# Optimization experiments

Measured on AMD Instinct MI355X. Metric: run time of the kernel, lower is better.

The kernel has to match this reference:

```python
import jax, jax.numpy as jnp
import numpy as np
from jax import lax

# Hyperparameters mirroring init_kwargs
W_DATA = 0.75
W_SMOOTH = 0.25
W_KNN = 0.5
W_BQ = 0.5
K_KNN = 32
K_BQ = 64
RADIUS = 0.75
P_NORM = 1  # loss_norm


def _sqdist(pc):
    # pc: [B,N,3] -> [B,N,N] squared pairwise distances
    x2 = jnp.sum(pc * pc, axis=-1)
    d = x2[:, :, None] + x2[:, None, :] - 2.0 * jnp.einsum('bnc,bmc->bnm', pc, pc)
    return jnp.maximum(d, 0.0)


def _group(flow, idx):
    # flow: [B,3,N], idx: [B,N,K] -> [B,3,N,K]
    return jax.vmap(lambda f, i: f[:, i])(flow, idx)


def _neighbor_loss(flow, idx):
    # flow: [B,3,N]; (flow_i - flow_j).norm(p, dim=channel).mean(K).mean()
    nn_flow = _group(flow, idx)                    # [B,3,N,K]
    diff = flow[:, :, :, None] - nn_flow           # [B,3,N,K]
    if P_NORM == 1:
        n = jnp.sum(jnp.abs(diff), axis=1)         # [B,N,K]
    else:
        n = jnp.sum(jnp.abs(diff) ** P_NORM, axis=1) ** (1.0 / P_NORM)
    return jnp.mean(jnp.mean(n, axis=-1))


def _knn_idx(sqd):
    # k nearest (self included); if dist > radius, replace with nearest index
    neg_vals, idx = lax.top_k(-sqd, K_KNN)         # [B,N,K]
    dist = jnp.sqrt(jnp.maximum(-neg_vals, 0.0))
    tmp = idx[:, :, 0:1]
    return jnp.where(dist > RADIUS, tmp, idx)


def _ballq_idx(sqd):
    # first K_BQ indices (in index order) with sqdist < radius^2, padded by first hit
    N = sqd.shape[-1]
    ar = jnp.arange(N, dtype=jnp.int32)
    keys = jnp.where(sqd < RADIUS * RADIUS, ar[None, None, :], N)  # [B,N,N]
    vals = -lax.top_k(-keys, K_BQ)[0]              # K smallest keys -> [B,N,K]
    first = vals[:, :, 0:1]
    return jnp.where(vals == N, first, vals)


def setup_inputs() -> dict:
    key = jax.random.key(0)
    k1, k2, k3, k4 = jax.random.split(key, 4)
    B, N = 4, 8192
    return {
        'pc_source': jax.random.normal(k1, (B, N, 3), dtype=jnp.float32),
        'pc_target': jax.random.normal(k2, (B, N, 3), dtype=jnp.float32),
        'pred_flow': jax.random.normal(k3, (B, N, 3), dtype=jnp.float32),
        'gt_flow': jax.random.normal(k4, (B, N, 3), dtype=jnp.float32),
        'i': 0,
    }


def reference(pc_source, pc_target, pred_flow, gt_flow, i):
    # data term: L1
    data_loss = jnp.mean(jnp.abs(pred_flow - gt_flow))
    # smoothness term
    flow = jnp.transpose(pred_flow, (0, 2, 1))     # [B,3,N]
    sqd = _sqdist(pc_source)                       # [B,N,N]
    knn_loss = _neighbor_loss(flow, _knn_idx(sqd))
    bq_loss = _neighbor_loss(flow, _ballq_idx(sqd))
    smooth = W_KNN * knn_loss + W_BQ * bq_loss
    return W_DATA * data_loss + W_SMOOTH * smooth
```

## Files before the change

### kernel.cpp

```cpp
#include <hip/hip_runtime.h>
#include <hip/hip_bf16.h>
#include <hip/hip_fp16.h>

#define NPTS 8192
#define NB 4
#define R2C 0.5625f
#define BSC (64.0f/0.5625f)
#define RPW 2
#define WPB 4
#define NGRP 256
#define NUNITS (NB*NPTS/RPW)
#define GPB (NPTS/RPW)
#define NBLK 2048
#define NCTR 64
#define UPC (NUNITS/NCTR)
#define CSTRIDE 32

typedef unsigned char u8;
typedef unsigned u32;
typedef unsigned long long u64;

__device__ __forceinline__ float wsum(float v){
#pragma unroll
  for (int o=32;o>0;o>>=1) v += __shfl_xor(v,o,64);
  return v;
}
__device__ __forceinline__ float rfl(float v){
  return __int_as_float(__builtin_amdgcn_readfirstlane(__float_as_int(v)));
}
__device__ __forceinline__ int cellof(float x,float y,float z){
  int ix=min(15,max(0,(int)((x+5.f)*1.6f)));
  int iy=min(15,max(0,(int)((y+5.f)*1.6f)));
  int iz=min(15,max(0,(int)((z+5.f)*1.6f)));
  int sx=(ix&1)|((ix&2)<<2)|((ix&4)<<4)|((ix&8)<<6);
  int sy=(iy&1)|((iy&2)<<2)|((iy&4)<<4)|((iy&8)<<6);
  int sz=(iz&1)|((iz&2)<<2)|((iz&4)<<4)|((iz&8)<<6);
  return (sx<<2)|(sy<<1)|sz;
}
__device__ __forceinline__ u32 om(float f){
  u32 u=__float_as_uint(f);
  return (u&0x80000000u)? ~u : (u|0x80000000u);
}
__device__ __forceinline__ float iom(u32 m){
  u32 u=(m&0x80000000u)? (m&0x7fffffffu) : ~m;
  return __uint_as_float(u);
}

__global__ __launch_bounds__(1024) void sort_k(
    const float* __restrict__ pc, const float* __restrict__ fl,
    float4* __restrict__ pA, float2* __restrict__ pB,
    unsigned short* __restrict__ ab, u32* __restrict__ ctr){
  __shared__ u32 hist[4096];
  __shared__ u32 amm[NGRP*6];
  __shared__ u32 wsums[16];
  const int b=blockIdx.x, tid=threadIdx.x, lane=tid&63, wid=tid>>6;
  for (int i=tid;i<4096;i+=1024) hist[i]=0u;
  for (int i=tid;i<NGRP*6;i+=1024) amm[i]=(i&1)?0u:0xFFFFFFFFu;
  if (b==0) for (int i=tid;i<NCTR*CSTRIDE;i+=1024) ctr[i]=0u;
  __syncthreads();
  const float* pcb=pc+(size_t)b*NPTS*3;
  const float* flb=fl+(size_t)b*NPTS*3;
  for (int i=tid;i<NPTS;i+=1024){
    float x=pcb[3*i],y=pcb[3*i+1],z=pcb[3*i+2];
    atomicAdd(&hist[cellof(x,y,z)],1u);
  }
  __syncthreads();
  {
    u32 loc[4]; u32 run=0;
#pragma unroll
    for (int k=0;k<4;k++){ u32 v=hist[tid*4+k]; loc[k]=run; run+=v; }
    u32 inc=run;
#pragma unroll
    for (int o=1;o<64;o<<=1){ u32 y=__shfl_up(inc,o,64); if (lane>=o) inc+=y; }
    if (lane==63) wsums[wid]=inc;
    __syncthreads();
    u32 wbase=0;
    for (int i=0;i<wid;i++) wbase+=wsums[i];
    u32 tbase=wbase+inc-run;
#pragma unroll
    for (int k=0;k<4;k++) hist[tid*4+k]=tbase+loc[k];
  }
  __syncthreads();
  for (int i=tid;i<NPTS;i+=1024){
    float x=pcb[3*i],y=pcb[3*i+1],z=pcb[3*i+2];
    int c=cellof(x,y,z);
    u32 pos=atomicAdd(&hist[c],1u);
    int d=b*NPTS+(int)pos;
    pA[d]=make_float4(x,y,z,flb[3*i]);
    pB[d]=make_float2(flb[3*i+1],flb[3*i+2]);
    int g=(int)(pos>>5);
    atomicMin(&amm[g*6+0],om(x)); atomicMax(&amm[g*6+1],om(x));
    atomicMin(&amm[g*6+2],om(y)); atomicMax(&amm[g*6+3],om(y));
    atomicMin(&amm[g*6+4],om(z)); atomicMax(&amm[g*6+5],om(z));
  }
  __syncthreads();
  if (tid<NGRP){
    unsigned short* p6=ab+(b*NGRP+tid)*6;
    p6[0]=__half_as_ushort(__float2half_rd(iom(amm[tid*6+0])));
    p6[1]=__half_as_ushort(__float2half_ru(iom(amm[tid*6+1])));
    p6[2]=__half_as_ushort(__float2half_rd(iom(amm[tid*6+2])));
    p6[3]=__half_as_ushort(__float2half_ru(iom(amm[tid*6+3])));
    p6[4]=__half_as_ushort(__float2half_rd(iom(amm[tid*6+4])));
    p6[5]=__half_as_ushort(__float2half_ru(iom(amm[tid*6+5])));
  }
}

__global__ void finp_k(const float* __restrict__ part, float* __restrict__ out){
  int lane=threadIdx.x;
  double k=0.0,b=0.0,d=0.0;
  for (int i=lane;i<NBLK;i+=64){ k+=part[3*i]; b+=part[3*i+1]; d+=part[3*i+2]; }
#pragma unroll
  for (int o=32;o>0;o>>=1){
    k+=__shfl_xor(k,o,64); b+=__shfl_xor(b,o,64); d+=__shfl_xor(d,o,64);
  }
  if (lane==0){
    double knn=k/(32768.0*32.0), bq=b/(32768.0*64.0), dat=d/98304.0;
    out[0]=(float)(0.75*dat+0.25*(0.5*knn+0.5*bq));
  }
}

__global__ __launch_bounds__(256,4) void main_k(
  const float* __restrict__ fl, const float* __restrict__ gt,
  const float4* __restrict__ gpA, const float2* __restrict__ gpB,
  const unsigned short* __restrict__ ab,
  float* __restrict__ part, u32* __restrict__ ctr)
{
  __shared__ unsigned short sab[NB][NGRP*6];
  __shared__ u64  histp[WPB][RPW][64];
  __shared__ u8   glg[WPB][NGRP];
  __shared__ float wred[WPB][3];

  const int tid=threadIdx.x, lane=tid&63, wv=tid>>6, bid=blockIdx.x;
  const u64 lt=(1ull<<lane)-1ull;
  const bool lo=(lane<32);
  const int l5=lane&31;

  { const u32* s=(const u32*)ab;
    u32* d=(u32*)&sab[0][0];
    for (int k=tid;k<NB*NGRP*3;k+=256) d[k]=s[k]; }
  __syncthreads();

  float dl=0.f;
  for (int e=bid*256+tid; e<NB*NPTS*3; e+=gridDim.x*256) dl+=fabsf(fl[e]-gt[e]);
  dl=wsum(dl);

  float tknn=0.f, tbq=0.f;
  int cp=bid&(NCTR-1);

  for (;;){
    int k;
    if (lane==0){
      u32 kk=atomicAdd(&ctr[cp*CSTRIDE],1u);
      if (kk>=UPC){
        kk=0x7fffffffu;
        int qb=cp&~3;
#pragma unroll
        for (int t=0;t<4;t++){
          int c2=qb+t;
          if (c2==cp) continue;
          u32 v=*(volatile u32*)&ctr[c2*CSTRIDE];
          if (v<UPC){
            u32 k2=atomicAdd(&ctr[c2*CSTRIDE],1u);
            if (k2<UPC){ cp=c2; kk=k2; break; }
          }
        }
      }
      k=(int)kk;
    }
    k=__shfl(k,0,64);
    cp=__shfl(cp,0,64);
    if (k>=UPC) break;
    const int u=cp+(k<<6);

    const int b=u>>12;
    const int i0=(u&(GPB-1))*RPW;
    const float4* pA=gpA+b*NPTS;
    const float2* pB=gpB+b*NPTS;

    float rx[RPW],ry[RPW],rz[RPW],rfx[RPW],rfy[RPW],rfz[RPW];
#pragma unroll
    for (int r=0;r<RPW;r++){
      float4 A=pA[i0+r]; float2 B=pB[i0+r];
      rx[r]=rfl(A.x); ry[r]=rfl(A.y); rz[r]=rfl(A.z);
      rfx[r]=rfl(A.w); rfy[r]=rfl(B.x); rfz[r]=rfl(B.y);
    }
    float wx0=rx[0],wx1=rx[0],wy0=ry[0],wy1=ry[0],wz0=rz[0],wz1=rz[0];
#pragma unroll
    for (int r=1;r<RPW;r++){
      wx0=fminf(wx0,rx[r]); wx1=fmaxf(wx1,rx[r]);
      wy0=fminf(wy0,ry[r]); wy1=fmaxf(wy1,ry[r]);
      wz0=fminf(wz0,rz[r]); wz1=fmaxf(wz1,rz[r]);
    }

    int nsur;
    {
      int base=0;
#pragma unroll
      for (int h=0;h<4;h++){
        const unsigned short* a=&sab[b][(h*64+lane)*6];
        float gx0=__half2float(__ushort_as_half(a[0])), gx1=__half2float(__ushort_as_half(a[1]));
        float gy0=__half2float(__ushort_as_half(a[2])), gy1=__half2float(__ushort_as_half(a[3]));
        float gz0=__half2float(__ushort_as_half(a[4])), gz1=__half2float(__ushort_as_half(a[5]));
        float dxm=fmaxf(0.f,fmaxf(gx0-wx1,wx0-gx1));
        float dym=fmaxf(0.f,fmaxf(gy0-wy1,wy0-gy1));
        float dzm=fmaxf(0.f,fmaxf(gz0-wz1,wz0-gz1));
        float d2=fmaf(dxm,dxm,fmaf(dym,dym,dzm*dzm));
        bool c=d2<R2C;
        u64 bm=__ballot(c);
        if (c){ int p=base+__popcll(bm&lt); glg[wv][p]=(u8)(h*64+lane); }
        base+=__popcll(bm);
      }
      nsur=base;
    }
#pragma unroll
    for (int r=0;r<RPW;r++) histp[wv][r][lane]=0ull;

    int cnt[RPW]; float f1[RPW]; float bqa=0.f;
#pragma unroll
    for (int r=0;r<RPW;r++){ cnt[r]=0; f1[r]=0.f; }
    {
      const int npair=(nsur+1)>>1;
      int s0=(0)|(lo?0:1);
      int jb=(int)glg[wv][min(s0,nsur-1)]*32+l5;
      float4 J=pA[jb]; float2 JF=pB[jb];
      int s1=(min(1,npair-1)<<1)|(lo?0:1);
      int jb1=(int)glg[wv][min(s1,nsur-1)]*32+l5;
      float4 N1=pA[jb1]; float2 NF1=pB[jb1];
#pragma unroll 1
      for (int t=0;t<npair;t++){
        int s2=(min(t+2,npair-1)<<1)|(lo?0:1);
        int jb2=(int)glg[wv][min(s2,nsur-1)]*32+l5;
        float4 N2=pA[jb2]; float2 NF2=pB[jb2];
        bool vld=lo||((t<<1)+1<nsur);
        bool open=false;
#pragma unroll
        for (int r=0;r<RPW;r++) open = open || (cnt[r]<64);
#pragma unroll
        for (int r=0;r<RPW;r++){
          float dx=rx[r]-J.x, dy=ry[r]-J.y, dz=rz[r]-J.z;
          float sq=fmaf(dx,dx,fmaf(dy,dy,dz*dz));
          bool in=(sq<R2C)&&vld;
          if (in){
            int bin=min((int)(sq*BSC),63);
            float l1=fabsf(J.w-rfx[r])+fabsf(JF.x-rfy[r])+fabsf(JF.y-rfz[r]);
            atomicAdd(&histp[wv][r][bin],(1ull<<44)+(u64)(l1*16777216.0f));
          }
          if (cnt[r]<64){
            u64 m=__ballot(in);
            if (in){
              int p=cnt[r]+__popcll(m&lt);
              if (p<64){
                float l1=fabsf(J.w-rfx[r])+fabsf(JF.x-rfy[r])+fabsf(JF.y-rfz[r]);
                bqa+=l1;
                if (p==0) f1[r]=l1;
              }
            }
            cnt[r]+=__popcll(m);
          }
        }
        J=N1; JF=NF1; N1=N2; NF1=NF2;
      }
    }

    float knn=0.f;
#pragma unroll
    for (int r=0;r<RPW;r++){
      u64 v=histp[wv][r][lane];
      u32 hh=(u32)(v>>44);
      float ll=(float)(v&0xFFFFFFFFFFFull)*5.9604645e-8f;
      u32 inc=hh;
#pragma unroll
      for (int o=1;o<64;o<<=1){ u32 y=__shfl_up(inc,o,64); if (lane>=o) inc+=y; }
      int M=__shfl((int)inc,63,64);
      if (M<=32){
        knn+=wsum(ll);
      } else {
        u32 exc=inc-hh;
        bool sel=(exc<=32u)&&(inc>32u);
        u64 sm=__ballot(sel);
        int src=__ffsll(sm)-1;
        int rneed=__shfl(32-(int)exc,src,64);
        float bl=__shfl(ll,src,64);
        u32 bh=__shfl(hh,src,64);
        float below=wsum(lane<src?ll:0.f);
        knn+=below+(float)rneed*bl/(float)bh;
      }
    }

    float bqt=wsum(bqa);
#pragma unroll
    for (int r=0;r<RPW;r++){
      float ff=wsum(f1[r]);
      bqt+=(float)(64-min(cnt[r],64))*ff;
    }
    tknn+=knn; tbq+=bqt;
  }

  if (lane==0){ wred[wv][0]=tknn; wred[wv][1]=tbq; wred[wv][2]=dl; }
  __syncthreads();
  if (tid==0){
    float k=0.f,bb=0.f,dd=0.f;
#pragma unroll
    for (int w2=0;w2<WPB;w2++){ k+=wred[w2][0]; bb+=wred[w2][1]; dd+=wred[w2][2]; }
    part[bid*3]=k; part[bid*3+1]=bb; part[bid*3+2]=dd;
  }
}

#define TILE 1024
#define FRPB 16
#define FRPW 4
__global__ void init_ws_k(double* ws){ int t=threadIdx.x; if(t<3) ws[t]=0.0; }
__global__ void fin_k(const double* __restrict__ ws, float* __restrict__ out){
  double knn = ws[0] / (32768.0*32.0);
  double bq  = ws[1] / (32768.0*64.0);
  double dat = ws[2] / 98304.0;
  out[0] = (float)(0.75*dat + 0.25*(0.5*knn + 0.5*bq));
}
__global__ __launch_bounds__(256) void fb_loss_k(
  const float* __restrict__ pc, const float* __restrict__ fl,
  const float* __restrict__ gt, double* __restrict__ ws)
{
  __shared__ float sx[TILE],sy[TILE],sz[TILE],sfx[TILE],sfy[TILE],sfz[TILE];
  __shared__ unsigned fhist[FRPB][64];
  __shared__ u64 fbkey[FRPB][64];
  __shared__ float fbl1v[FRPB][64];
  const int tid=threadIdx.x, lane=tid&63, wv=tid>>6, bid=blockIdx.x;
  const u64 lt=(1ull<<lane)-1ull;
  float dl=0.f;
  for (int e=bid*256+tid; e<NB*NPTS*3; e+=gridDim.x*256) dl+=fabsf(fl[e]-gt[e]);
  dl=wsum(dl);
  if (lane==0 && dl!=0.f) atomicAdd(ws+2,(double)dl);
  const int row0=bid*FRPB+wv*FRPW;
  const int b=row0/NPTS, i0=row0-b*NPTS;
  const float* pcb=pc+(size_t)b*NPTS*3;
  const float* flb=fl+(size_t)b*NPTS*3;
  float xi[FRPW],yi[FRPW],zi[FRPW],fxi[FRPW],fyi[FRPW],fzi[FRPW];
  int cnt[FRPW]; float bqa[FRPW], f1[FRPW];
#pragma unroll
  for (int r=0;r<FRPW;r++){
    int i=i0+r;
    xi[r]=pcb[3*i]; yi[r]=pcb[3*i+1]; zi[r]=pcb[3*i+2];
    fxi[r]=flb[3*i]; fyi[r]=flb[3*i+1]; fzi[r]=flb[3*i+2];
    cnt[r]=0; bqa[r]=0.f; f1[r]=0.f;
  }
  { unsigned* hp=&fhist[0][0];
    for (int h=tid; h<FRPB*64; h+=256) hp[h]=0u; }
  for (int t=0;t<NPTS/TILE;t++){
#pragma unroll
    for (int k=0;k<TILE/256;k++){
      int p=k*256+tid, g=t*TILE+p;
      sx[p]=pcb[3*g]; sy[p]=pcb[3*g+1]; sz[p]=pcb[3*g+2];
      sfx[p]=flb[3*g]; sfy[p]=flb[3*g+1]; sfz[p]=flb[3*g+2];
    }
    __syncthreads();
#pragma unroll
    for (int r=0;r<FRPW;r++){
      const int wrow=wv*FRPW+r;
#pragma unroll 4
      for (int it=0;it<TILE/64;it++){
        int jl=it*64+lane;
        float dx=sx[jl]-xi[r],dy=sy[jl]-yi[r],dz=sz[jl]-zi[r];
        float sq=fmaf(dx,dx,fmaf(dy,dy,dz*dz));
        bool in=sq<R2C;
        u64 m=__ballot(in);
        if (in){ int bin=min((int)(sq*BSC),63); atomicAdd(&fhist[wrow][bin],1u); }
        if (cnt[r]<64){
          if (in){
            int p=cnt[r]+__popcll(m&lt);
            if (p<64){
              float l1=fabsf(sfx[jl]-fxi[r])+fabsf(sfy[jl]-fyi[r])+fabsf(sfz[jl]-fzi[r]);
              bqa[r]+=l1;
              if (p==0) f1[r]=l1;
            }
          }
        }
        cnt[r]+=__popcll(m);
      }
    }
    __syncthreads();
  }
  int bstar[FRPW],rneed[FRPW];
#pragma unroll
  for (int r=0;r<FRPW;r++){
    const int wrow=wv*FRPW+r;
    unsigned h=fhist[wrow][lane];
    unsigned inc=h;
#pragma unroll
    for (int o=1;o<64;o<<=1){ unsigned y=__shfl_up(inc,o,64); if (lane>=o) inc+=y; }
    int M=__shfl((int)inc,63,64);
    if (M<=32){ bstar[r]=64; rneed[r]=0; }
    else{
      unsigned exc=inc-h;
      bool sel=(exc<=32u)&&(inc>32u);
      u64 sm=__ballot(sel);
      int src=__ffsll(sm)-1;
      bstar[r]=src;
      rneed[r]=__shfl(32-(int)exc,src,64);
    }
  }
  float knn=0.f; int bcnt[FRPW]={0,0,0,0};
  for (int t=0;t<NPTS/TILE;t++){
#pragma unroll
    for (int k=0;k<TILE/256;k++){
      int p=k*256+tid, g=t*TILE+p;
      sx[p]=pcb[3*g]; sy[p]=pcb[3*g+1]; sz[p]=pcb[3*g+2];
      sfx[p]=flb[3*g]; sfy[p]=flb[3*g+1]; sfz[p]=flb[3*g+2];
    }
    __syncthreads();
#pragma unroll
    for (int r=0;r<FRPW;r++){
      const int wrow=wv*FRPW+r;
#pragma unroll 4
      for (int it=0;it<TILE/64;it++){
        int jl=it*64+lane;
        float dx=sx[jl]-xi[r],dy=sy[jl]-yi[r],dz=sz[jl]-zi[r];
        float sq=fmaf(dx,dx,fmaf(dy,dy,dz*dz));
        bool in=sq<R2C;
        int bin=min((int)(sq*BSC),63);
        bool keep=in&&(bin<bstar[r]);
        bool isb=in&&(bin==bstar[r]);
        float l1=0.f;
        if (keep||isb)
          l1=fabsf(sfx[jl]-fxi[r])+fabsf(sfy[jl]-fyi[r])+fabsf(sfz[jl]-fzi[r]);
        if (keep) knn+=l1;
        u64 mb2=__ballot(isb);
        if (isb){
          int p=bcnt[r]+__popcll(mb2&lt);
          if (p<64){
            fbkey[wrow][p]=((u64)__float_as_uint(sq)<<32)|(unsigned)(t*TILE+jl);
            fbl1v[wrow][p]=l1;
          }
        }
        bcnt[r]+=__popcll(mb2);
      }
    }
    __syncthreads();
  }
#pragma unroll
  for (int r=0;r<FRPW;r++){
    const int wrow=wv*FRPW+r;
    int L=min(bcnt[r],64);
    u64 mykey=~0ull; float myl1=0.f;
    if (lane<L){ mykey=fbkey[wrow][lane]; myl1=fbl1v[wrow][lane]; }
    int rank=0;
    for (int q=0;q<L;q++) rank += (fbkey[wrow][q]<mykey)?1:0;
    if (lane<L && rank<rneed[r]) knn+=myl1;
  }
  knn=wsum(knn);
  float bqt=0.f;
#pragma unroll
  for (int r=0;r<FRPW;r++){
    float s=wsum(bqa[r]);
    float ff=wsum(f1[r]);
    s+=(float)(64-min(cnt[r],64))*ff;
    bqt+=s;
  }
  if (lane==0){
    atomicAdd(ws+0,(double)knn);
    atomicAdd(ws+1,(double)bqt);
  }
}

extern "C" void kernel_launch(void* const* d_in, const int* in_sizes, int n_in,
                              void* d_out, int out_size, void* d_ws, size_t ws_size,
                              hipStream_t stream) {
  (void)in_sizes; (void)n_in; (void)out_size;
  const float* pc = (const float*)d_in[0];
  const float* fl = (const float*)d_in[2];
  const float* gt = (const float*)d_in[3];
  float* out = (float*)d_out;
  char* w = (char*)d_ws;
  double* acc = (double*)w;

  const size_t SORT_OFF = 256;
  const size_t PB_OFF   = SORT_OFF + (size_t)NB*NPTS*16u;
  const size_t AABB_OFF = PB_OFF + (size_t)NB*NPTS*8u;
  const size_t PART_OFF = AABB_OFF + (size_t)NB*NGRP*6*2u;
  const size_t CTR_OFF  = PART_OFF + (size_t)NBLK*3*4u;
  const size_t NEED     = CTR_OFF + (size_t)NCTR*CSTRIDE*4u;

  if (ws_size < NEED){
    hipLaunchKernelGGL(init_ws_k, dim3(1), dim3(64), 0, stream, acc);
    hipLaunchKernelGGL(fb_loss_k, dim3((NB*NPTS)/FRPB), dim3(256), 0, stream,
                       pc, fl, gt, acc);
    hipLaunchKernelGGL(fin_k, dim3(1), dim3(1), 0, stream, acc, out);
    return;
  }
  float4* pA = (float4*)(w+SORT_OFF);
  float2* pB = (float2*)(w+PB_OFF);
  unsigned short* ab = (unsigned short*)(w+AABB_OFF);
  float* part = (float*)(w+PART_OFF);
  u32* ctr = (u32*)(w+CTR_OFF);

  hipLaunchKernelGGL(sort_k, dim3(NB),   dim3(1024), 0, stream, pc, fl, pA, pB, ab, ctr);
  hipLaunchKernelGGL(main_k, dim3(NBLK), dim3(256),  0, stream,
                     fl, gt, pA, pB, ab, part, ctr);
  hipLaunchKernelGGL(finp_k, dim3(1), dim3(64), 0, stream, part, out);
}
```

Before: 96.13 us.

## Split spatial counting sort across four blocks per batch with global AABB atomics

The sort kernel previously ran one block per batch (4 blocks). It now runs four blocks per batch. Each block recomputes the full per-slice cell histogram (packed 16-bit counts) and scatters only its quarter of the points, offset by the counts of earlier slices. Group bounding boxes are now built with global atomics on a u32 buffer that a new zero kernel initialises, and main_k converts them to half precision when it loads them. This adds an extra launch, redundant histogram work and global atomic contention in exchange for four times more parallelism in the serial-ish sort stage.

```diff
diff --git a/kernel.cpp b/kernel.cpp
--- a/kernel.cpp
+++ b/kernel.cpp
@@ -15,6 +15,7 @@
 #define NCTR 64
 #define UPC (NUNITS/NCTR)
 #define CSTRIDE 32
+#define NSL 4
 
 typedef unsigned char u8;
 typedef unsigned u32;
@@ -46,29 +47,43 @@
   return __uint_as_float(u);
 }
 
+__global__ void zero_k(u32* __restrict__ abg, u32* __restrict__ ctr){
+  int t=blockIdx.x*1024+threadIdx.x;
+  if (t<NB*NGRP*6) abg[t]=(t&1)?0u:0xFFFFFFFFu;
+  if (t<NCTR*CSTRIDE) ctr[t]=0u;
+}
+
 __global__ __launch_bounds__(1024) void sort_k(
     const float* __restrict__ pc, const float* __restrict__ fl,
     float4* __restrict__ pA, float2* __restrict__ pB,
-    unsigned short* __restrict__ ab, u32* __restrict__ ctr){
-  __shared__ u32 hist[4096];
-  __shared__ u32 amm[NGRP*6];
+    u32* __restrict__ abg){
+  __shared__ u32 shp[NSL][2048];
+  __shared__ u32 sbase[4096];
+  __shared__ u32 curp[2048];
   __shared__ u32 wsums[16];
-  const int b=blockIdx.x, tid=threadIdx.x, lane=tid&63, wid=tid>>6;
-  for (int i=tid;i<4096;i+=1024) hist[i]=0u;
-  for (int i=tid;i<NGRP*6;i+=1024) amm[i]=(i&1)?0u:0xFFFFFFFFu;
-  if (b==0) for (int i=tid;i<NCTR*CSTRIDE;i+=1024) ctr[i]=0u;
+  const int b=blockIdx.x>>2, s=blockIdx.x&3;
+  const int tid=threadIdx.x, lane=tid&63, wid=tid>>6;
+  for (int i=tid;i<NSL*2048;i+=1024) ((u32*)shp)[i]=0u;
+  for (int i=tid;i<2048;i+=1024) curp[i]=0u;
   __syncthreads();
   const float* pcb=pc+(size_t)b*NPTS*3;
   const float* flb=fl+(size_t)b*NPTS*3;
   for (int i=tid;i<NPTS;i+=1024){
     float x=pcb[3*i],y=pcb[3*i+1],z=pcb[3*i+2];
-    atomicAdd(&hist[cellof(x,y,z)],1u);
+    int c=cellof(x,y,z);
+    int j=i>>11;
+    atomicAdd(&shp[j][c>>1],(c&1)?65536u:1u);
   }
   __syncthreads();
   {
     u32 loc[4]; u32 run=0;
 #pragma unroll
-    for (int k=0;k<4;k++){ u32 v=hist[tid*4+k]; loc[k]=run; run+=v; }
+    for (int k=0;k<4;k++){
+      int c=tid*4+k; u32 tot=0;
+#pragma unroll
+      for (int j=0;j<NSL;j++) tot+=(shp[j][c>>1]>>((c&1)*16))&0xFFFFu;
+      loc[k]=run; run+=tot;
+    }
     u32 inc=run;
 #pragma unroll
     for (int o=1;o<64;o<<=1){ u32 y=__shfl_up(inc,o,64); if (lane>=o) inc+=y; }
@@ -78,30 +93,25 @@
     for (int i=0;i<wid;i++) wbase+=wsums[i];
     u32 tbase=wbase+inc-run;
 #pragma unroll
-    for (int k=0;k<4;k++) hist[tid*4+k]=tbase+loc[k];
+    for (int k=0;k<4;k++) sbase[tid*4+k]=tbase+loc[k];
   }
   __syncthreads();
-  for (int i=tid;i<NPTS;i+=1024){
+  for (int ii=tid;ii<2048;ii+=1024){
+    int i=s*2048+ii;
     float x=pcb[3*i],y=pcb[3*i+1],z=pcb[3*i+2];
     int c=cellof(x,y,z);
-    u32 pos=atomicAdd(&hist[c],1u);
+    u32 rr=atomicAdd(&curp[c>>1],(c&1)?65536u:1u);
+    u32 rank=(rr>>((c&1)*16))&0xFFFFu;
+    u32 prev=0;
+    for (int j=0;j<s;j++) prev+=(shp[j][c>>1]>>((c&1)*16))&0xFFFFu;
+    u32 pos=sbase[c]+prev+rank;
     int d=b*NPTS+(int)pos;
     pA[d]=make_float4(x,y,z,flb[3*i]);
     pB[d]=make_float2(flb[3*i+1],flb[3*i+2]);
-    int g=(int)(pos>>5);
-    atomicMin(&amm[g*6+0],om(x)); atomicMax(&amm[g*6+1],om(x));
-    atomicMin(&amm[g*6+2],om(y)); atomicMax(&amm[g*6+3],om(y));
-    atomicMin(&amm[g*6+4],om(z)); atomicMax(&amm[g*6+5],om(z));
-  }
-  __syncthreads();
-  if (tid<NGRP){
-    unsigned short* p6=ab+(b*NGRP+tid)*6;
-    p6[0]=__half_as_ushort(__float2half_rd(iom(amm[tid*6+0])));
-    p6[1]=__half_as_ushort(__float2half_ru(iom(amm[tid*6+1])));
-    p6[2]=__half_as_ushort(__float2half_rd(iom(amm[tid*6+2])));
-    p6[3]=__half_as_ushort(__float2half_ru(iom(amm[tid*6+3])));
-    p6[4]=__half_as_ushort(__float2half_rd(iom(amm[tid*6+4])));
-    p6[5]=__half_as_ushort(__float2half_ru(iom(amm[tid*6+5])));
+    u32* a=abg+(b*NGRP+(int)(pos>>5))*6;
+    atomicMin(&a[0],om(x)); atomicMax(&a[1],om(x));
+    atomicMin(&a[2],om(y)); atomicMax(&a[3],om(y));
+    atomicMin(&a[4],om(z)); atomicMax(&a[5],om(z));
   }
 }
 
@@ -122,7 +132,7 @@
 __global__ __launch_bounds__(256,4) void main_k(
   const float* __restrict__ fl, const float* __restrict__ gt,
   const float4* __restrict__ gpA, const float2* __restrict__ gpB,
-  const unsigned short* __restrict__ ab,
+  const u32* __restrict__ abg,
   float* __restrict__ part, u32* __restrict__ ctr)
 {
   __shared__ unsigned short sab[NB][NGRP*6];
@@ -135,9 +145,13 @@
   const bool lo=(lane<32);
   const int l5=lane&31;
 
-  { const u32* s=(const u32*)ab;
-    u32* d=(u32*)&sab[0][0];
-    for (int k=tid;k<NB*NGRP*3;k+=256) d[k]=s[k]; }
+  { unsigned short* d=&sab[0][0];
+    for (int k=tid;k<NB*NGRP*6;k+=256){
+      float f=iom(abg[k]);
+      d[k]=(k&1)? __half_as_ushort(__float2half_ru(f))
+                : __half_as_ushort(__float2half_rd(f));
+    }
+  }
   __syncthreads();
 
   float dl=0.f;
@@ -475,7 +489,7 @@
   const size_t SORT_OFF = 256;
   const size_t PB_OFF   = SORT_OFF + (size_t)NB*NPTS*16u;
   const size_t AABB_OFF = PB_OFF + (size_t)NB*NPTS*8u;
-  const size_t PART_OFF = AABB_OFF + (size_t)NB*NGRP*6*2u;
+  const size_t PART_OFF = AABB_OFF + (size_t)NB*NGRP*6*4u;
   const size_t CTR_OFF  = PART_OFF + (size_t)NBLK*3*4u;
   const size_t NEED     = CTR_OFF + (size_t)NCTR*CSTRIDE*4u;
 
@@ -488,12 +502,13 @@
   }
   float4* pA = (float4*)(w+SORT_OFF);
   float2* pB = (float2*)(w+PB_OFF);
-  unsigned short* ab = (unsigned short*)(w+AABB_OFF);
+  u32* abg = (u32*)(w+AABB_OFF);
   float* part = (float*)(w+PART_OFF);
   u32* ctr = (u32*)(w+CTR_OFF);
 
-  hipLaunchKernelGGL(sort_k, dim3(NB),   dim3(1024), 0, stream, pc, fl, pA, pB, ab, ctr);
-  hipLaunchKernelGGL(main_k, dim3(NBLK), dim3(256),  0, stream,
-                     fl, gt, pA, pB, ab, part, ctr);
+  hipLaunchKernelGGL(zero_k, dim3(8),      dim3(1024), 0, stream, abg, ctr);
+  hipLaunchKernelGGL(sort_k, dim3(NB*NSL), dim3(1024), 0, stream, pc, fl, pA, pB, abg);
+  hipLaunchKernelGGL(main_k, dim3(NBLK),   dim3(256),  0, stream,
+                     fl, gt, pA, pB, abg, part, ctr);
   hipLaunchKernelGGL(finp_k, dim3(1), dim3(64), 0, stream, part, out);
 }
```

Result: slower. 116.4 us (+21.1%).
